# Kernel optimization log

Measured on AMD Instinct MI355X. Metric: run time of the kernel, lower is better.

Reference implementation:

```python
import jax, jax.numpy as jnp
import numpy as np

NC = 10          # tess_size (number of tessellation cells on [0,1])
D = NC - 1       # CPA parameter dim with zero boundary
EPS = 1e-7
N = 2097152      # number of 2D points
MASK = jnp.array([1, 0])  # left=True coupling mask

def _make_basis(nc):
    # Continuous piecewise-affine velocity on [0,1]: cell c has v(x)=a_c*x+b_c.
    # Constraints: continuity at interior knots + zero boundary v(0)=v(1)=0.
    L = np.zeros((nc + 1, 2 * nc))
    for k in range(1, nc):
        xk = k / nc
        L[k - 1, 2 * (k - 1)] = xk; L[k - 1, 2 * (k - 1) + 1] = 1.0
        L[k - 1, 2 * k] = -xk;      L[k - 1, 2 * k + 1] = -1.0
    L[nc - 1, 1] = 1.0                                        # v(0) = 0
    L[nc, 2 * (nc - 1)] = 1.0; L[nc, 2 * (nc - 1) + 1] = 1.0  # v(1) = 0
    _, _, Vt = np.linalg.svd(L)
    return jnp.asarray(Vt[nc + 1:].T, dtype=jnp.float32)      # (2*nc, D) null-space basis (svd)

_B = _make_basis(NC)

def cpab_flow(x, theta):
    """Integrate dphi/dt = v(phi), t in [0,1], v CPA parameterized by theta.
    x: (N,1) in [0,1], theta: (N,D). Returns (phi(x,1), dphi/dx), each (N,1).
    Closed-form per-cell integration with cell hopping (<= NC hops, fixed scan).
    dphi/dx = exp(sum_c a_c * dt_c) (analytic space gradient)."""
    A = (theta @ _B.T).reshape(-1, NC, 2)          # (N, NC, 2): (a_c, b_c)
    xp = x[:, 0]
    c0 = jnp.clip((xp * NC).astype(jnp.int32), 0, NC - 1)
    carry0 = (xp, jnp.ones_like(xp), c0, jnp.zeros_like(xp))

    def step(carry, _):
        phi, t, c, ld = carry
        a = jnp.take_along_axis(A[:, :, 0], c[:, None], 1)[:, 0]
        b = jnp.take_along_axis(A[:, :, 1], c[:, None], 1)[:, 0]
        v = a * phi + b
        lin = jnp.abs(a) < 1e-10
        sa = jnp.where(lin, 1.0, a)
        xc = jnp.where(v >= 0, (c + 1).astype(phi.dtype), c.astype(phi.dtype)) / NC
        den = phi + b / sa
        den = jnp.where(jnp.abs(den) < 1e-30, 1e-30, den)
        t_exp = jnp.log(jnp.maximum((xc + b / sa) / den, 1e-30)) / sa
        sb = jnp.where(jnp.abs(b) < 1e-30, 1.0, b)
        thit = jnp.where(lin, (xc - phi) / sb, t_exp)
        thit = jnp.where(jnp.abs(v) < 1e-14, jnp.inf, thit)   # fixed point: never leaves cell
        cross = thit < t
        dt = jnp.where(cross, thit, t)
        phi_new = jnp.where(lin, phi + b * dt,
                            (phi + b / sa) * jnp.exp(a * dt) - b / sa)
        phi_new = jnp.where(cross, xc, phi_new)               # snap to knot when hopping
        active = t > 0
        phi = jnp.where(active, phi_new, phi)
        ld = ld + jnp.where(active, a * dt, 0.0)              # accumulate log dphi/dx
        t = jnp.where(active, t - dt, t)
        c = jnp.where(active & cross,
                      jnp.clip(c + jnp.where(v >= 0, 1, -1), 0, NC - 1), c)
        return (phi, t, c, ld), None

    (phi, _, _, ld), _ = jax.lax.scan(step, carry0, None, length=NC)
    return phi[:, None], jnp.exp(ld)[:, None]

def mlp(h, p):
    # Linear -> (Linear, ReLU) x 2 -> Linear  (matches torch MLP(hidden_layers=3))
    h = h @ p[0] + p[1]
    h = jax.nn.relu(h @ p[2] + p[3])
    h = jax.nn.relu(h @ p[4] + p[5])
    return h @ p[6] + p[7]

def setup_inputs():
    key = jax.random.key(0)
    ks = jax.random.split(key, 17)
    inp = {"x": jax.random.uniform(ks[0], (N, 2), dtype=jnp.float32)}
    shapes = [(1, 10), (10,), (10, 10), (10,), (10, 10), (10,), (10, D), (D,)]
    names = ["w0", "b0", "w1", "b1", "w2", "b2", "w3", "b3"]
    i = 1
    for pref in ("m1", "m2"):
        for nm, sh in zip(names, shapes):
            scale = 0.3 if len(sh) == 2 else 0.1
            inp[pref + nm] = jax.random.normal(ks[i], sh, dtype=jnp.float32) * scale
            i += 1
    return inp

def reference(x, m1w0, m1b0, m1w1, m1b1, m1w2, m1b2, m1w3, m1b3,
              m2w0, m2b0, m2w1, m2b1, m2w2, m2b2, m2w3, m2b3):
    x = jnp.clip(x, EPS, 1.0 - EPS)
    xs = x[:, MASK]                        # index_select with coupling mask
    x1, x2 = xs[:, 0:1], xs[:, 1:2]
    theta2 = mlp(x1, (m2w0, m2b0, m2w1, m2b1, m2w2, m2b2, m2w3, m2b3))
    z2, g2 = cpab_flow(x2, theta2)
    theta1 = mlp(z2, (m1w0, m1b0, m1w1, m1b1, m1w2, m1b2, m1w3, m1b3))
    z1, g1 = cpab_flow(x1, theta1)
    z = jnp.concatenate([z1, z2], axis=1)[:, MASK]
    log_dz_dx = jnp.log(jnp.concatenate([g1, g2], axis=1))[:, MASK]
    return z, log_dz_dx
```

## Files before the change

### kernel.cpp

```cpp
#include <hip/hip_runtime.h>
#include <cmath>

#define THREADS 256
#define NCELL 10
#define DDIM 9

#define LN2F 0.69314718056f
#define K10L 14.426950408889634f
#define LIN_THR_L 1.442695e-10f

typedef float f32x2 __attribute__((ext_vector_type(2)));

__device__ __forceinline__ f32x2 fma2(f32x2 a, f32x2 b, f32x2 c) {
  return __builtin_elementwise_fma(a, b, c);
}
__device__ __forceinline__ f32x2 max2(f32x2 a, f32x2 b) {
  return __builtin_elementwise_max(a, b);
}

struct Basis { float Bt[DDIM][2 * NCELL]; };

static void compute_basis_host(Basis* bs) {
  double L[11][20];
  for (int r = 0; r < 11; ++r)
    for (int c = 0; c < 20; ++c) L[r][c] = 0.0;
  for (int k = 1; k < NCELL; ++k) {
    double xk = (double)k / (double)NCELL;
    L[k - 1][2 * (k - 1)] = xk;
    L[k - 1][2 * (k - 1) + 1] = 1.0;
    L[k - 1][2 * k] = -xk;
    L[k - 1][2 * k + 1] = -1.0;
  }
  L[NCELL - 1][1] = 1.0;
  L[NCELL][2 * (NCELL - 1)] = 1.0;
  L[NCELL][2 * (NCELL - 1) + 1] = 1.0;

  double v[11][20];
  double tau[11];
  for (int i = 0; i < 11; ++i) {
    double alpha = L[i][i];
    double xn2 = 0.0;
    for (int l = i + 1; l < 20; ++l) xn2 += L[i][l] * L[i][l];
    double xnorm = sqrt(xn2);
    for (int l = 0; l < 20; ++l) v[i][l] = 0.0;
    v[i][i] = 1.0;
    if (xnorm == 0.0) {
      tau[i] = 0.0;
    } else {
      double beta = sqrt(alpha * alpha + xn2);
      if (alpha >= 0.0) beta = -beta;
      tau[i] = (beta - alpha) / beta;
      double sc = 1.0 / (alpha - beta);
      for (int l = i + 1; l < 20; ++l) v[i][l] = L[i][l] * sc;
      L[i][i] = beta;
      for (int j = i + 1; j < 11; ++j) {
        double w = 0.0;
        for (int l = i; l < 20; ++l) w += L[j][l] * v[i][l];
        w *= tau[i];
        for (int l = i; l < 20; ++l) L[j][l] -= w * v[i][l];
      }
    }
  }
  for (int j = 11; j < 20; ++j) {
    double q[20];
    for (int l = 0; l < 20; ++l) q[l] = 0.0;
    q[j] = 1.0;
    for (int i = 10; i >= 0; --i) {
      double w = 0.0;
      for (int l = i; l < 20; ++l) w += v[i][l] * q[l];
      w *= tau[i];
      for (int l = i; l < 20; ++l) q[l] -= w * v[i][l];
    }
    for (int l = 0; l < 20; ++l) bs->Bt[j - 11][l] = (float)q[l];
  }
}

__global__ void fold_kernel(
    const float* __restrict__ w0_1, const float* __restrict__ b0_1,
    const float* __restrict__ w1_1, const float* __restrict__ b1_1,
    const float* __restrict__ w3_1, const float* __restrict__ b3_1,
    const float* __restrict__ w0_2, const float* __restrict__ b0_2,
    const float* __restrict__ w1_2, const float* __restrict__ b1_2,
    const float* __restrict__ w3_2, const float* __restrict__ b3_2,
    float* __restrict__ ws, Basis bb) {
  for (int f = threadIdx.x; f < 260; f += THREADS) {
    int m = f / 130;
    int j = f % 130;
    const float* w0 = (m == 0) ? w0_1 : w0_2;
    const float* b0 = (m == 0) ? b0_1 : b0_2;
    const float* w1 = (m == 0) ? w1_1 : w1_2;
    const float* w3 = (m == 0) ? w3_1 : w3_2;
    const float* b3 = (m == 0) ? b3_1 : b3_2;
    const float* b1 = (m == 0) ? b1_1 : b1_2;
    float val = 0.0f;
    if (j < 10) {
      for (int r = 0; r < 10; ++r) val += w0[r] * w1[r * 10 + j];
    } else if (j < 20) {
      int jj = j - 10;
      for (int r = 0; r < 10; ++r) val += b0[r] * w1[r * 10 + jj];
      val += b1[jj];
    } else if (j < 120) {
      int jj = j - 20;
      int r = jj / 10, k = jj % 10;
      if (k < 9) {
        float g = (float)(k + 1) * 0.1f;
        for (int t = 0; t < DDIM; ++t)
          val += w3[r * DDIM + t] * (bb.Bt[t][2 * (k + 1)] * g + bb.Bt[t][2 * (k + 1) + 1]);
      }
    } else {
      int k = j - 120;
      if (k < 9) {
        float g = (float)(k + 1) * 0.1f;
        for (int t = 0; t < DDIM; ++t)
          val += b3[t] * (bb.Bt[t][2 * (k + 1)] * g + bb.Bt[t][2 * (k + 1) + 1]);
      }
    }
    ws[f] = val;
  }
}

__device__ __forceinline__ void mlp_A(float xin,
    const float* __restrict__ w2, const float* __restrict__ b2,
    const float* __restrict__ wbf,
    f32x2* abcol, float& aminL, float& bmin) {
  const f32x2* W01 = (const f32x2*)wbf;
  const f32x2* B01 = W01 + 5;
  const f32x2* W3V = W01 + 10;
  const f32x2* B3V = W01 + 60;
  const f32x2* w2p = (const f32x2*)w2;
  const f32x2* b2p = (const f32x2*)b2;

  f32x2 h1[5], h2[5];
  f32x2 xx = {xin, xin};
  f32x2 zero = {0.0f, 0.0f};
#pragma unroll
  for (int p = 0; p < 5; ++p) h1[p] = max2(fma2(xx, W01[p], B01[p]), zero);

#pragma unroll
  for (int p = 0; p < 5; ++p) h2[p] = b2p[p];
#pragma unroll
  for (int r = 0; r < 10; ++r) {
    float h = h1[r >> 1][r & 1];
    f32x2 hh = {h, h};
#pragma unroll
    for (int p = 0; p < 5; ++p) h2[p] = fma2(hh, w2p[r * 5 + p], h2[p]);
  }
#pragma unroll
  for (int p = 0; p < 5; ++p) h2[p] = max2(h2[p], zero);

  f32x2 vp[5];
#pragma unroll
  for (int p = 0; p < 5; ++p) vp[p] = B3V[p];
#pragma unroll
  for (int r = 0; r < 10; ++r) {
    float h = h2[r >> 1][r & 1];
    f32x2 hh = {h, h};
#pragma unroll
    for (int p = 0; p < 5; ++p) vp[p] = fma2(hh, W3V[r * 5 + p], vp[p]);
  }

  float v[NCELL + 1];
  v[0] = 0.0f;
#pragma unroll
  for (int k = 1; k <= NCELL; ++k) v[k] = vp[(k - 1) >> 1][(k - 1) & 1];

  float amn = 1e30f, bmn = 1e30f;
#pragma unroll
  for (int c = 0; c < NCELL; ++c) {
    float aL = (v[c + 1] - v[c]) * K10L;
    f32x2 ab; ab[0] = aL; ab[1] = v[c];
    abcol[c * THREADS] = ab;
    amn = fminf(amn, fabsf(aL));
    if (c >= 1) bmn = fminf(bmn, fabsf(v[c]));
  }
  aminL = amn;
  bmin = bmn;
}

__device__ __forceinline__ void flow_fast(float x0, const f32x2* abcol,
                                          int c0, float aL0, float v0,
                                          float& zo, float& ldo) {
  bool right = (v0 >= 0.0f);
  float d01L = right ? 0.1f * LN2F : -0.1f * LN2F;
  int dirI = right ? 1 : -1;
  float c0f = (float)c0;
  float xc0 = (right ? c0f + 1.0f : c0f) * 0.1f;

  float rv0 = __builtin_amdgcn_rcpf(v0);
  float rv = rv0;
  float aL = aL0;
  float raL = __builtin_amdgcn_rcpf(aL);
  float ventry = v0;
  float t = 1.0f;
  int c = c0;
  bool cross;

  int cn = c + dirI; cn = cn < 0 ? 0 : (cn > 9 ? 9 : cn);
  float aLn = abcol[cn * THREADS][0];
  float ran = __builtin_amdgcn_rcpf(aLn);

  {
    float dxL = (xc0 - x0) * LN2F;
    float vxc = fmaf(aL, dxL, ventry);
    float ratio = fmaxf(vxc * rv, 1e-30f);
    float thit = __log2f(ratio) * raL;
    cross = thit < t;
    t = cross ? t - thit : t;
    ventry = cross ? vxc : ventry;
    float rvn = __builtin_amdgcn_rcpf(vxc);
    rv = cross ? rvn : rv;
    aL = cross ? aLn : aL;
    raL = cross ? ran : raL;
    c = cross ? cn : c;
  }
  if (!__all(!cross)) {
    cn = c + dirI; cn = cn < 0 ? 0 : (cn > 9 ? 9 : cn);
    aLn = abcol[cn * THREADS][0];
    ran = __builtin_amdgcn_rcpf(aLn);
    for (int it = 1; it < NCELL; ++it) {
      float vxc = fmaf(aL, d01L, ventry);
      float ratio = fmaxf(vxc * rv, 1e-30f);
      float thit = __log2f(ratio) * raL;
      cross = cross && (thit < t);
      t = cross ? t - thit : t;
      ventry = cross ? vxc : ventry;
      float rvn = __builtin_amdgcn_rcpf(vxc);
      rv = cross ? rvn : rv;
      aL = cross ? aLn : aL;
      raL = cross ? ran : raL;
      c = cross ? cn : c;
      if (__all(!cross)) break;
      cn = c + dirI; cn = cn < 0 ? 0 : (cn > 9 ? 9 : cn);
      aLn = abcol[cn * THREADS][0];
      ran = __builtin_amdgcn_rcpf(aLn);
    }
  }
  float aF = aL * LN2F;
  bool moved = t != 1.0f;
  float ceF = (float)(right ? c : c + 1) * 0.1f;
  float x_e = moved ? ceF : x0;
  float bF = fmaf(-aF, x_e, ventry);
  float rsa = __builtin_amdgcn_rcpf(aF);
  float bsa = bF * rsa;
  float E = __expf(aF * t);
  float z = fmaf(x_e + bsa, E, -bsa);
  bool done = !cross;
  z = done ? z : x_e;
  float ld = __logf(fmaxf(ventry * rv0, 1e-30f));
  ld += done ? aF * t : 0.0f;
  zo = z;
  ldo = ld;
}

__device__ __noinline__ void flow_slow(float x0, const f32x2* abcol,
                                       int c0, float aL0, float v0,
                                       float& zo, float& ldo) {
  bool right = (v0 >= 0.0f);
  float d01 = right ? 0.1f : -0.1f;
  int dirI = right ? 1 : -1;
  float a = aL0 * LN2F;
  float b = fmaf(-a, (float)c0 * 0.1f, abcol[c0 * THREADS][1]);
  float xc = (float)(right ? (c0 + 1) : c0) * 0.1f;
  float rv0 = __builtin_amdgcn_rcpf(v0);
  float rv = rv0;
  bool tiny = fabsf(v0) < 1e-14f;
  bool lin = fabsf(a) < 1e-10f;
  float ra = __builtin_amdgcn_rcpf(lin ? 1.0f : a);
  float phiC = x0;
  float t = 1.0f;
  bool cross = false;
  int c = c0;

  int cn = c + dirI; cn = cn < 0 ? 0 : (cn > 9 ? 9 : cn);
  f32x2 sn = abcol[cn * THREADS];
  float an = sn[0] * LN2F;
  float bn = fmaf(-an, (float)cn * 0.1f, sn[1]);
  bool linn = fabsf(an) < 1e-10f;
  float ran = __builtin_amdgcn_rcpf(linn ? 1.0f : an);

  for (int it = 0; it < NCELL; ++it) {
    float vxc = fmaf(a, xc, b);
    float ratio = fmaxf(vxc * rv, 1e-30f);
    float l = __logf(ratio);
    float thit = l * ra;
    if (lin) {
      float sb = (fabsf(b) < 1e-30f) ? 1.0f : b;
      thit = (xc - phiC) * __builtin_amdgcn_rcpf(sb);
    }
    thit = tiny ? __builtin_inff() : thit;
    bool crN = (thit < t);
    cross = (it == 0) ? crN : (cross && crN);
    t = cross ? (t - thit) : t;
    phiC = cross ? xc : phiC;
    float rvn = __builtin_amdgcn_rcpf(vxc);
    rv = cross ? rvn : rv;
    tiny = cross ? (fabsf(vxc) < 1e-14f) : tiny;
    a = cross ? an : a;
    b = cross ? bn : b;
    lin = cross ? linn : lin;
    ra = cross ? ran : ra;
    xc = cross ? (xc + d01) : xc;
    c = cross ? cn : c;
    if (__all(!cross)) break;
    cn = c + dirI; cn = cn < 0 ? 0 : (cn > 9 ? 9 : cn);
    sn = abcol[cn * THREADS];
    an = sn[0] * LN2F;
    bn = fmaf(-an, (float)cn * 0.1f, sn[1]);
    linn = fabsf(an) < 1e-10f;
    ran = __builtin_amdgcn_rcpf(linn ? 1.0f : an);
  }
  bool done = !cross;
  float vterm = fmaf(a, phiC, b);
  float ld = __logf(fmaxf(vterm * rv0, 1e-30f));
  bool linf = fabsf(a) < 1e-10f;
  float rsaf = __builtin_amdgcn_rcpf(linf ? 1.0f : a);
  float bsa = b * rsaf;
  float E = __expf(a * t);
  float pnl = fmaf(phiC + bsa, E, -bsa);
  float pli = fmaf(b, t, phiC);
  float p1 = linf ? pli : pnl;
  zo = done ? p1 : phiC;
  ldo = ld + (done ? a * t : 0.0f);
}

__device__ __forceinline__ void flow_dev(float x0, const f32x2* abcol,
                                         float aminL, float bmin,
                                         float& zo, float& ldo) {
  int c0 = (int)(x0 * 10.0f);
  c0 = c0 < 0 ? 0 : (c0 > 9 ? 9 : c0);
  f32x2 s0 = abcol[c0 * THREADS];
  float aL0 = s0[0], vL0 = s0[1];
  float dxL = (x0 - (float)c0 * 0.1f) * LN2F;
  float v0 = fmaf(aL0, dxL, vL0);
  bool risky = (aminL < LIN_THR_L) || (bmin < 1e-12f) || (fabsf(v0) < 1e-12f);
  if (__any(risky)) {
    flow_slow(x0, abcol, c0, aL0, v0, zo, ldo);
  } else {
    flow_fast(x0, abcol, c0, aL0, v0, zo, ldo);
  }
}

__global__ __launch_bounds__(THREADS, 4) void cpab2d_kernel(
    const float* __restrict__ x,
    const float* __restrict__ m1w2, const float* __restrict__ m1b2,
    const float* __restrict__ m2w2, const float* __restrict__ m2b2,
    const float* __restrict__ wsf,
    float* __restrict__ out, int n) {
  __shared__ f32x2 AB[NCELL][THREADS];
  int i = blockIdx.x * THREADS + threadIdx.x;
  if (i >= n) return;

  float2 xi = reinterpret_cast<const float2*>(x)[i];
  float x2v = fminf(fmaxf(xi.x, 1e-7f), 1.0f - 1e-7f);
  float x1v = fminf(fmaxf(xi.y, 1e-7f), 1.0f - 1e-7f);

  f32x2* abcol = &AB[0][threadIdx.x];
  float aminL, bmin;

  mlp_A(x1v, m2w2, m2b2, wsf + 130, abcol, aminL, bmin);
  float z2, ld2;
  flow_dev(x2v, abcol, aminL, bmin, z2, ld2);

  mlp_A(z2, m1w2, m1b2, wsf, abcol, aminL, bmin);
  float z1, ld1;
  flow_dev(x1v, abcol, aminL, bmin, z1, ld1);

  reinterpret_cast<float2*>(out)[i] = make_float2(z2, z1);
  reinterpret_cast<float2*>(out + 2 * (size_t)n)[i] = make_float2(ld2, ld1);
}

extern "C" void kernel_launch(void* const* d_in, const int* in_sizes, int n_in,
                              void* d_out, int out_size, void* d_ws, size_t ws_size,
                              hipStream_t stream) {
  const float* x    = (const float*)d_in[0];
  const float* m1w0 = (const float*)d_in[1];
  const float* m1b0 = (const float*)d_in[2];
  const float* m1w1 = (const float*)d_in[3];
  const float* m1b1 = (const float*)d_in[4];
  const float* m1w2 = (const float*)d_in[5];
  const float* m1b2 = (const float*)d_in[6];
  const float* m1w3 = (const float*)d_in[7];
  const float* m1b3 = (const float*)d_in[8];
  const float* m2w0 = (const float*)d_in[9];
  const float* m2b0 = (const float*)d_in[10];
  const float* m2w1 = (const float*)d_in[11];
  const float* m2b1 = (const float*)d_in[12];
  const float* m2w2 = (const float*)d_in[13];
  const float* m2b2 = (const float*)d_in[14];
  const float* m2w3 = (const float*)d_in[15];
  const float* m2b3 = (const float*)d_in[16];
  float* out = (float*)d_out;
  float* wsf = (float*)d_ws;
  int n = in_sizes[0] / 2;

  Basis bs;
  compute_basis_host(&bs);

  fold_kernel<<<1, THREADS, 0, stream>>>(
      m1w0, m1b0, m1w1, m1b1, m1w3, m1b3,
      m2w0, m2b0, m2w1, m2b1, m2w3, m2b3, wsf, bs);

  dim3 grid((n + THREADS - 1) / THREADS), block(THREADS);
  cpab2d_kernel<<<grid, block, 0, stream>>>(
      x, m1w2, m1b2, m2w2, m2b2, wsf, out, n);
}
```

Measured before the change: 42.91 us.

## Store slope reciprocals in LDS, track |v|, use raw hardware log2/exp2

The per-cell LDS table now holds the slope and its reciprocal instead of slope and knot velocity. The starting cell's slope and velocity are computed in registers inside the MLP epilogue, so the initial LDS read goes away. The fast path tracks the speed magnitude so the log ratio stays positive without clamping. It uses raw v_log_f32/v_exp_f32 asm and reuses the reciprocal, removing reciprocals per hop and at the end. The slow path rebuilds the intercept from the entry velocity, and the asm intrinsics skip denormal handling, which slightly changes precision.

```diff
diff --git a/kernel.cpp b/kernel.cpp
--- a/kernel.cpp
+++ b/kernel.cpp
@@ -6,6 +6,7 @@
 #define DDIM 9
 
 #define LN2F 0.69314718056f
+#define RLN2F 1.4426950408889634f
 #define K10L 14.426950408889634f
 #define LIN_THR_L 1.442695e-10f
 
@@ -16,6 +17,12 @@
 }
 __device__ __forceinline__ f32x2 max2(f32x2 a, f32x2 b) {
   return __builtin_elementwise_max(a, b);
+}
+__device__ __forceinline__ float log2_hw(float x) {
+  float r; asm("v_log_f32 %0, %1" : "=v"(r) : "v"(x)); return r;
+}
+__device__ __forceinline__ float exp2_hw(float x) {
+  float r; asm("v_exp_f32 %0, %1" : "=v"(r) : "v"(x)); return r;
 }
 
 struct Basis { float Bt[DDIM][2 * NCELL]; };
@@ -122,7 +129,8 @@
 __device__ __forceinline__ void mlp_A(float xin,
     const float* __restrict__ w2, const float* __restrict__ b2,
     const float* __restrict__ wbf,
-    f32x2* abcol, float& aminL, float& bmin) {
+    f32x2* alcol, int c0, float xflow,
+    float& aL0, float& raL0, float& v0, float& aminL, float& bmin) {
   const f32x2* W01 = (const f32x2*)wbf;
   const f32x2* B01 = W01 + 5;
   const f32x2* W3V = W01 + 10;
@@ -165,101 +173,105 @@
   for (int k = 1; k <= NCELL; ++k) v[k] = vp[(k - 1) >> 1][(k - 1) & 1];
 
   float amn = 1e30f, bmn = 1e30f;
+  float vs = v[0], vh = v[1];
 #pragma unroll
   for (int c = 0; c < NCELL; ++c) {
     float aL = (v[c + 1] - v[c]) * K10L;
-    f32x2 ab; ab[0] = aL; ab[1] = v[c];
-    abcol[c * THREADS] = ab;
+    f32x2 s; s[0] = aL; s[1] = __builtin_amdgcn_rcpf(aL);
+    alcol[c * THREADS] = s;
     amn = fminf(amn, fabsf(aL));
-    if (c >= 1) bmn = fminf(bmn, fabsf(v[c]));
+    if (c >= 1) {
+      bmn = fminf(bmn, fabsf(v[c]));
+      bool e = (c0 == c);
+      vs = e ? v[c] : vs;
+      vh = e ? v[c + 1] : vh;
+    }
   }
   aminL = amn;
   bmin = bmn;
-}
-
-__device__ __forceinline__ void flow_fast(float x0, const f32x2* abcol,
-                                          int c0, float aL0, float v0,
+  aL0 = (vh - vs) * K10L;
+  raL0 = __builtin_amdgcn_rcpf(aL0);
+  v0 = fmaf(aL0, (xflow - (float)c0 * 0.1f) * LN2F, vs);
+}
+
+__device__ __forceinline__ void flow_fast(float x0, const f32x2* alcol,
+                                          int c0, float aL0, float raL0, float v0,
                                           float& zo, float& ldo) {
   bool right = (v0 >= 0.0f);
-  float d01L = right ? 0.1f * LN2F : -0.1f * LN2F;
   int dirI = right ? 1 : -1;
-  float c0f = (float)c0;
-  float xc0 = (right ? c0f + 1.0f : c0f) * 0.1f;
-
-  float rv0 = __builtin_amdgcn_rcpf(v0);
-  float rv = rv0;
-  float aL = aL0;
-  float raL = __builtin_amdgcn_rcpf(aL);
-  float ventry = v0;
+  float xc0 = (float)(right ? c0 + 1 : c0) * 0.1f;
+  const float C01 = 0.1f * LN2F;
+
+  float u = fabsf(v0);
+  float ru = __builtin_amdgcn_rcpf(u);
+  float ru0 = ru;
+  float aL = aL0, raL = raL0;
   float t = 1.0f;
   int c = c0;
   bool cross;
 
   int cn = c + dirI; cn = cn < 0 ? 0 : (cn > 9 ? 9 : cn);
-  float aLn = abcol[cn * THREADS][0];
-  float ran = __builtin_amdgcn_rcpf(aLn);
+  f32x2 sn = alcol[cn * THREADS];
 
   {
-    float dxL = (xc0 - x0) * LN2F;
-    float vxc = fmaf(aL, dxL, ventry);
-    float ratio = fmaxf(vxc * rv, 1e-30f);
-    float thit = __log2f(ratio) * raL;
+    float dxL = fabsf(xc0 - x0) * LN2F;
+    float uxc = fmaf(aL, dxL, u);
+    float l2 = log2_hw(uxc * ru);
+    float thit = l2 * raL;
     cross = thit < t;
     t = cross ? t - thit : t;
-    ventry = cross ? vxc : ventry;
-    float rvn = __builtin_amdgcn_rcpf(vxc);
-    rv = cross ? rvn : rv;
-    aL = cross ? aLn : aL;
-    raL = cross ? ran : raL;
+    float run = __builtin_amdgcn_rcpf(uxc);
+    u = cross ? uxc : u;
+    ru = cross ? run : ru;
+    aL = cross ? sn[0] : aL;
+    raL = cross ? sn[1] : raL;
     c = cross ? cn : c;
   }
   if (!__all(!cross)) {
     cn = c + dirI; cn = cn < 0 ? 0 : (cn > 9 ? 9 : cn);
-    aLn = abcol[cn * THREADS][0];
-    ran = __builtin_amdgcn_rcpf(aLn);
+    sn = alcol[cn * THREADS];
     for (int it = 1; it < NCELL; ++it) {
-      float vxc = fmaf(aL, d01L, ventry);
-      float ratio = fmaxf(vxc * rv, 1e-30f);
-      float thit = __log2f(ratio) * raL;
+      float uxc = fmaf(aL, C01, u);
+      float l2 = log2_hw(uxc * ru);
+      float thit = l2 * raL;
       cross = cross && (thit < t);
       t = cross ? t - thit : t;
-      ventry = cross ? vxc : ventry;
-      float rvn = __builtin_amdgcn_rcpf(vxc);
-      rv = cross ? rvn : rv;
-      aL = cross ? aLn : aL;
-      raL = cross ? ran : raL;
+      float run = __builtin_amdgcn_rcpf(uxc);
+      u = cross ? uxc : u;
+      ru = cross ? run : ru;
+      aL = cross ? sn[0] : aL;
+      raL = cross ? sn[1] : raL;
       c = cross ? cn : c;
       if (__all(!cross)) break;
       cn = c + dirI; cn = cn < 0 ? 0 : (cn > 9 ? 9 : cn);
-      aLn = abcol[cn * THREADS][0];
-      ran = __builtin_amdgcn_rcpf(aLn);
+      sn = alcol[cn * THREADS];
     }
   }
   float aF = aL * LN2F;
   bool moved = t != 1.0f;
   float ceF = (float)(right ? c : c + 1) * 0.1f;
   float x_e = moved ? ceF : x0;
+  float sgn = right ? 1.0f : -1.0f;
+  float ventry = u * sgn;
   float bF = fmaf(-aF, x_e, ventry);
-  float rsa = __builtin_amdgcn_rcpf(aF);
-  float bsa = bF * rsa;
-  float E = __expf(aF * t);
+  float bsa = bF * (raL * RLN2F);
+  float E = exp2_hw(aL * t);
   float z = fmaf(x_e + bsa, E, -bsa);
   bool done = !cross;
   z = done ? z : x_e;
-  float ld = __logf(fmaxf(ventry * rv0, 1e-30f));
+  float ld = LN2F * log2_hw(u * ru0);
   ld += done ? aF * t : 0.0f;
   zo = z;
   ldo = ld;
 }
 
-__device__ __noinline__ void flow_slow(float x0, const f32x2* abcol,
-                                       int c0, float aL0, float v0,
+__device__ __noinline__ void flow_slow(float x0, const f32x2* alcol,
+                                       int c0, float a0, float v0,
                                        float& zo, float& ldo) {
   bool right = (v0 >= 0.0f);
   float d01 = right ? 0.1f : -0.1f;
   int dirI = right ? 1 : -1;
-  float a = aL0 * LN2F;
-  float b = fmaf(-a, (float)c0 * 0.1f, abcol[c0 * THREADS][1]);
+  float a = a0;
   float xc = (float)(right ? (c0 + 1) : c0) * 0.1f;
   float rv0 = __builtin_amdgcn_rcpf(v0);
   float rv = rv0;
@@ -267,23 +279,24 @@
   bool lin = fabsf(a) < 1e-10f;
   float ra = __builtin_amdgcn_rcpf(lin ? 1.0f : a);
   float phiC = x0;
+  float ventry = v0;
   float t = 1.0f;
   bool cross = false;
   int c = c0;
 
   int cn = c + dirI; cn = cn < 0 ? 0 : (cn > 9 ? 9 : cn);
-  f32x2 sn = abcol[cn * THREADS];
+  f32x2 sn = alcol[cn * THREADS];
   float an = sn[0] * LN2F;
-  float bn = fmaf(-an, (float)cn * 0.1f, sn[1]);
   bool linn = fabsf(an) < 1e-10f;
   float ran = __builtin_amdgcn_rcpf(linn ? 1.0f : an);
 
   for (int it = 0; it < NCELL; ++it) {
-    float vxc = fmaf(a, xc, b);
+    float vxc = fmaf(a, xc - phiC, ventry);
     float ratio = fmaxf(vxc * rv, 1e-30f);
     float l = __logf(ratio);
     float thit = l * ra;
     if (lin) {
+      float b = fmaf(-a, phiC, ventry);
       float sb = (fabsf(b) < 1e-30f) ? 1.0f : b;
       thit = (xc - phiC) * __builtin_amdgcn_rcpf(sb);
     }
@@ -294,24 +307,23 @@
     phiC = cross ? xc : phiC;
     float rvn = __builtin_amdgcn_rcpf(vxc);
     rv = cross ? rvn : rv;
+    ventry = cross ? vxc : ventry;
     tiny = cross ? (fabsf(vxc) < 1e-14f) : tiny;
     a = cross ? an : a;
-    b = cross ? bn : b;
     lin = cross ? linn : lin;
     ra = cross ? ran : ra;
     xc = cross ? (xc + d01) : xc;
     c = cross ? cn : c;
     if (__all(!cross)) break;
     cn = c + dirI; cn = cn < 0 ? 0 : (cn > 9 ? 9 : cn);
-    sn = abcol[cn * THREADS];
+    sn = alcol[cn * THREADS];
     an = sn[0] * LN2F;
-    bn = fmaf(-an, (float)cn * 0.1f, sn[1]);
     linn = fabsf(an) < 1e-10f;
     ran = __builtin_amdgcn_rcpf(linn ? 1.0f : an);
   }
   bool done = !cross;
-  float vterm = fmaf(a, phiC, b);
-  float ld = __logf(fmaxf(vterm * rv0, 1e-30f));
+  float ld = __logf(fmaxf(ventry * rv0, 1e-30f));
+  float b = fmaf(-a, phiC, ventry);
   bool linf = fabsf(a) < 1e-10f;
   float rsaf = __builtin_amdgcn_rcpf(linf ? 1.0f : a);
   float bsa = b * rsaf;
@@ -323,21 +335,21 @@
   ldo = ld + (done ? a * t : 0.0f);
 }
 
-__device__ __forceinline__ void flow_dev(float x0, const f32x2* abcol,
+__device__ __forceinline__ void flow_dev(float x0, const f32x2* alcol,
+                                         int c0, float aL0, float raL0, float v0,
                                          float aminL, float bmin,
                                          float& zo, float& ldo) {
-  int c0 = (int)(x0 * 10.0f);
-  c0 = c0 < 0 ? 0 : (c0 > 9 ? 9 : c0);
-  f32x2 s0 = abcol[c0 * THREADS];
-  float aL0 = s0[0], vL0 = s0[1];
-  float dxL = (x0 - (float)c0 * 0.1f) * LN2F;
-  float v0 = fmaf(aL0, dxL, vL0);
   bool risky = (aminL < LIN_THR_L) || (bmin < 1e-12f) || (fabsf(v0) < 1e-12f);
   if (__any(risky)) {
-    flow_slow(x0, abcol, c0, aL0, v0, zo, ldo);
+    flow_slow(x0, alcol, c0, aL0 * LN2F, v0, zo, ldo);
   } else {
-    flow_fast(x0, abcol, c0, aL0, v0, zo, ldo);
-  }
+    flow_fast(x0, alcol, c0, aL0, raL0, v0, zo, ldo);
+  }
+}
+
+__device__ __forceinline__ int cell_of(float x) {
+  int c = (int)(x * 10.0f);
+  return c < 0 ? 0 : (c > 9 ? 9 : c);
 }
 
 __global__ __launch_bounds__(THREADS, 4) void cpab2d_kernel(
@@ -346,7 +358,7 @@
     const float* __restrict__ m2w2, const float* __restrict__ m2b2,
     const float* __restrict__ wsf,
     float* __restrict__ out, int n) {
-  __shared__ f32x2 AB[NCELL][THREADS];
+  __shared__ f32x2 AL2[NCELL][THREADS];
   int i = blockIdx.x * THREADS + threadIdx.x;
   if (i >= n) return;
 
@@ -354,16 +366,18 @@
   float x2v = fminf(fmaxf(xi.x, 1e-7f), 1.0f - 1e-7f);
   float x1v = fminf(fmaxf(xi.y, 1e-7f), 1.0f - 1e-7f);
 
-  f32x2* abcol = &AB[0][threadIdx.x];
-  float aminL, bmin;
-
-  mlp_A(x1v, m2w2, m2b2, wsf + 130, abcol, aminL, bmin);
+  f32x2* alcol = &AL2[0][threadIdx.x];
+  float aL0, raL0, v0, aminL, bmin;
+
+  int c0a = cell_of(x2v);
+  mlp_A(x1v, m2w2, m2b2, wsf + 130, alcol, c0a, x2v, aL0, raL0, v0, aminL, bmin);
   float z2, ld2;
-  flow_dev(x2v, abcol, aminL, bmin, z2, ld2);
-
-  mlp_A(z2, m1w2, m1b2, wsf, abcol, aminL, bmin);
+  flow_dev(x2v, alcol, c0a, aL0, raL0, v0, aminL, bmin, z2, ld2);
+
+  int c0b = cell_of(x1v);
+  mlp_A(z2, m1w2, m1b2, wsf, alcol, c0b, x1v, aL0, raL0, v0, aminL, bmin);
   float z1, ld1;
-  flow_dev(x1v, abcol, aminL, bmin, z1, ld1);
+  flow_dev(x1v, alcol, c0b, aL0, raL0, v0, aminL, bmin, z1, ld1);
 
   reinterpret_cast<float2*>(out)[i] = make_float2(z2, z1);
   reinterpret_cast<float2*>(out + 2 * (size_t)n)[i] = make_float2(ld2, ld1);
```

New measurement: 45.97 us. 1.07x slower.
